# Performance work log

Hardware: AMD Instinct MI355X
Metric: run time of the kernel (lower is better)

## Reference

```python
import jax, jax.numpy as jnp
import numpy as np

N_BIT = 4
GROUP = 128
ALPHA_W = 1.0   # group_size > -1 forces weight alpha to 1.0
ALPHA_A = 0.9   # searched input alpha
TOKENS, D_IN, D_OUT = 2048, 2048, 2048


def _int_grid(n_bit):
    B = n_bit - 1
    v = [0.0] + [float(s * i) for i in range(1, 2 ** B) for s in (1, -1)]
    v = np.sort(np.asarray(v, np.float32)) * (32.0 / 2 ** B)
    return v


def _outlier_grid(n_bit, exp_bit=2, exp_base=5):
    B = n_bit - 1
    mant_bit = B - exp_bit
    vals = []
    for i in range(exp_base, exp_base + 2 ** exp_bit):
        for j in range(2 ** mant_bit):
            if i == exp_base and j == 0:
                continue
            v = 2.0 ** i * (1.0 + 2.0 ** (-mant_bit) * j)
            vals += [v, -v]
    return np.sort(np.asarray(vals, np.float32))


_QG = _int_grid(N_BIT)
MAX_Q = float(_QG.max())              # 28.0 for 4-bit int grid
MERGED_GRID = jnp.asarray(np.concatenate([_QG, _outlier_grid(N_BIT)]))  # [29]


def get_quant(x, alpha, group_size):
    """Faithful jax port of get_quant(): per-group scale, nearest merged-grid
    quantization, roll-based outlier/victim masking, fp16 dequant."""
    org_shape = x.shape
    if group_size == -2:
        t = x.reshape(-1)
        mean, std = t.mean(), t.std(ddof=1)
    else:
        t = x.reshape(-1, group_size) if group_size > 0 else x
        mean = t.mean(axis=1, keepdims=True)
        std = t.std(axis=1, ddof=1, keepdims=True)
    normal_max = jnp.maximum(jnp.abs(mean + 3 * std), jnp.abs(mean - 3 * std))
    scales = normal_max * alpha / MAX_Q
    # nearest grid point over merged quant+outlier grid (the chunk loop in the
    # original is memory-chunking only; math is identical done whole)
    labels = jnp.argmin(jnp.abs((t / scales)[..., None] - MERGED_GRID), axis=-1)
    qf = MERGED_GRID[labels].reshape(-1)
    # victim masking: outliers (|q|>32) steal their paired neighbor's slot
    mask = jnp.abs(qf) > 32.0
    victim_odd = jnp.roll(mask, 1).at[::2].set(False)
    victim_even = jnp.roll(mask & ~victim_odd, -1).at[1::2].set(False)
    qf = jnp.where(victim_odd | victim_even, 0.0, qf)
    if group_size >= -1:
        qf = qf.reshape(t.shape)
    deq = (qf * scales).astype(jnp.float16)
    return deq.reshape(org_shape)


def setup_inputs() -> dict:
    key = jax.random.key(0)
    k1, k2 = jax.random.split(key)
    x = jax.random.normal(k1, (TOKENS, D_IN), dtype=jnp.float32)
    weight = jax.random.normal(k2, (D_OUT, D_IN), dtype=jnp.float32) * 0.02
    return {"x": x, "weight": weight}


def reference(x, weight):
    # runtime path of OliVe_Linear.forward (post-calibration), group_size=128
    w_deq = get_quant(weight, ALPHA_W, GROUP).astype(jnp.float32)
    x_deq = get_quant(x, ALPHA_A, GROUP).astype(jnp.float32)
    return x_deq @ w_deq.T  # [tokens, out_features]
```

## Files before the change

kernel.cpp:

```cpp
#include <hip/hip_runtime.h>
#include <hip/hip_fp16.h>
#include <stdint.h>

#define TOKENS 2048
#define DIM    2048
#define GROUP  128
#define NGK    16

typedef _Float16 half_t;
typedef __attribute__((ext_vector_type(4)))  _Float16 f16x4;
typedef __attribute__((ext_vector_type(8)))  _Float16 f16x8;
typedef __attribute__((ext_vector_type(4)))  int   i32x4;
typedef __attribute__((ext_vector_type(16))) int   i32x16;
typedef __attribute__((ext_vector_type(4)))  float f32x4;
typedef __attribute__((ext_vector_type(16))) float f32x16;


__device__ __forceinline__ float group32_sum(float v) {
#pragma unroll
  for (int off = 16; off > 0; off >>= 1)
    v += __shfl_xor(v, off, 64);
  return v;
}

__device__ __forceinline__ float nearest_q4(float u) {
  float qi = fminf(fmaxf(rintf(u), -7.f), 7.f);
  float a = fabsf(u);
  float m = a <= 14.f ? 12.f : a <= 20.f ? 16.f : a <= 28.f ? 24.f
          : a <= 40.f ? 32.f : a <= 56.f ? 48.f : a <= 80.f ? 64.f : 96.f;
  float qo = copysignf(m, u);
  return (fabsf(u - qo) < fabsf(u - qi)) ? qo : qi;
}

__global__ __launch_bounds__(256) void quant2_kernel(
    const float* __restrict__ x, const float* __restrict__ w,
    int8_t* __restrict__ q8,
    half_t* __restrict__ ssxT,
    half_t* __restrict__ sswT) {
  const int wid  = threadIdx.x >> 6;
  const int lane = threadIdx.x & 63;
  const int l    = lane & 31;
  const int g    = blockIdx.x * 8 + wid * 2 + (lane >> 5);
  const int NG1  = TOKENS * DIM / GROUP;

  const float alpha = (g < NG1) ? 0.9f : 1.0f;
  const float* src  = (g < NG1) ? x : w;
  const int grow    = (g < NG1) ? g : g - NG1;
  const size_t sbase = (size_t)grow * GROUP + l * 4;

  const float4 v = *reinterpret_cast<const float4*>(src + sbase);

  const float mean = group32_sum(v.x + v.y + v.z + v.w) * (1.0f / 128.0f);
  const float d0 = v.x - mean, d1 = v.y - mean, d2 = v.z - mean, d3 = v.w - mean;
  const float var = group32_sum(d0 * d0 + d1 * d1 + d2 * d2 + d3 * d3) *
                    (1.0f / 127.0f);
  const float scale = (fabsf(mean) + 3.0f * sqrtf(var)) * alpha / 28.0f;
  const float rs4 = 0.25f / scale;

  float q0 = nearest_q4(v.x * rs4);
  float q1 = nearest_q4(v.y * rs4);
  float q2 = nearest_q4(v.z * rs4);
  float q3 = nearest_q4(v.w * rs4);
  if (fabsf(q0) > 8.0f)      q1 = 0.0f;
  else if (fabsf(q1) > 8.0f) q0 = 0.0f;
  if (fabsf(q2) > 8.0f)      q3 = 0.0f;
  else if (fabsf(q3) > 8.0f) q2 = 0.0f;

  const int p = ((int)q0 & 255) | (((int)q1 & 255) << 8) |
                (((int)q2 & 255) << 16) | (((int)q3 & 255) << 24);
  reinterpret_cast<int*>(q8)[(size_t)g * 32 + l] = p;

  if (l == 0) {
    const half_t ss = (half_t)(4.0f * scale);
    if (g < NG1) ssxT[(grow & 15) * 2048 + (grow >> 4)] = ss;
    else         sswT[(grow & 15) * 2048 + (grow >> 4)] = ss;
  }
}


__device__ __forceinline__ void gload_lds16(const int8_t* g, char* l) {
  __builtin_amdgcn_global_load_lds(
      (__attribute__((address_space(1))) uint32_t*)g,
      (__attribute__((address_space(3))) uint32_t*)l, 16, 0, 0);
}

__global__ __launch_bounds__(256, 2) void gemm_kernel(
    const int8_t* __restrict__ Aq, const int8_t* __restrict__ Bq,
    const half_t* __restrict__ ssxT, const half_t* __restrict__ sswT,
    float* __restrict__ C) {
  __shared__ char lds_raw[3 * 24576 + 6144];
  half_t* ssx_l = (half_t*)(lds_raw + 73728);
  half_t* ssw_l = (half_t*)(lds_raw + 73728 + 4096);

  const int tid  = threadIdx.x;
  const int lane = tid & 63;
  const int wid  = tid >> 6;
  const int wr   = wid >> 1;
  const int wc   = wid & 1;
  const int r31  = lane & 31;
  const int hi   = lane >> 5;

  const int bid = blockIdx.x;
  const int c   = bid & 7;
  const int idx = bid >> 3;
  const int bm  = ((c & 3) << 2) + (idx >> 4);
  const int bn  = ((c >> 2) << 4) + (idx & 15);

  const int8_t* gA = Aq + (size_t)(bm * 128) * DIM;
  const int8_t* gB = Bq + (size_t)(bn * 64) * DIM;

  auto stage = [&](char* buf, int g) {
#pragma unroll
    for (int i = 0; i < 4; ++i) {
      int P   = (i * 256 + tid) * 16;
      int row = P >> 7;
      int cb  = (P & 127) ^ ((row & 7) << 4);
      gload_lds16(gA + (size_t)row * DIM + g * 128 + cb, buf + P);
    }
#pragma unroll
    for (int i = 0; i < 2; ++i) {
      int P   = (i * 256 + tid) * 16;
      int row = P >> 7;
      int cb  = (P & 127) ^ ((row & 7) << 4);
      gload_lds16(gB + (size_t)row * DIM + g * 128 + cb, buf + 16384 + P);
    }
  };

  {
    int f = tid * 8;
    *reinterpret_cast<f16x8*>(&ssx_l[f]) =
        *reinterpret_cast<const f16x8*>(&ssxT[(f >> 7) * 2048 + bm * 128 + (f & 127)]);
  }
  if (tid < 128) {
    int f = tid * 8;
    *reinterpret_cast<f16x8*>(&ssw_l[f]) =
        *reinterpret_cast<const f16x8*>(&sswT[(f >> 6) * 2048 + bn * 64 + (f & 63)]);
  }
  __syncthreads();

  f32x16 accf[2] = {};
  const i32x16 zacc = {};

  auto compute = [&](const char* buf, int gk) {
    const char* cA = buf;
    const char* cB = buf + 16384;
    i32x16 acci[2];
#pragma unroll
    for (int ks = 0; ks < 4; ++ks) {
      const int cb = ks * 32 + hi * 16;
      i32x4 af[2], bf;
#pragma unroll
      for (int mt = 0; mt < 2; ++mt) {
        int row = wr * 64 + mt * 32 + r31;
        int pc  = cb ^ ((row & 7) << 4);
        af[mt] = *reinterpret_cast<const i32x4*>(cA + (row << 7) + pc);
      }
      {
        int row = wc * 32 + r31;
        int pc  = cb ^ ((row & 7) << 4);
        bf = *reinterpret_cast<const i32x4*>(cB + (row << 7) + pc);
      }
      __builtin_amdgcn_s_setprio(1);
#pragma unroll
      for (int mt = 0; mt < 2; ++mt)
        acci[mt] = __builtin_amdgcn_mfma_i32_32x32x32_i8(
            af[mt], bf, ks == 0 ? zacc : acci[mt], 0, 0, 0);
      __builtin_amdgcn_s_setprio(0);
    }
    const float sw = (float)ssw_l[gk * 64 + wc * 32 + r31];
#pragma unroll
    for (int mt = 0; mt < 2; ++mt)
#pragma unroll
      for (int q = 0; q < 4; ++q) {
        f16x4 sxh = *reinterpret_cast<const f16x4*>(
            &ssx_l[gk * 128 + wr * 64 + mt * 32 + 8 * q + 4 * hi]);
#pragma unroll
        for (int e = 0; e < 4; ++e)
          accf[mt][q * 4 + e] +=
              (float)sxh[e] * (sw * (float)acci[mt][q * 4 + e]);
      }
  };

  char* S0 = lds_raw;
  char* S1 = lds_raw + 24576;
  char* S2 = lds_raw + 49152;

  stage(S0, 0);
  stage(S1, 1);

  auto iter = [&](int j, const char* cbuf, char* sbuf) {
    if (j <= 13) {
      stage(sbuf, j + 2);
      asm volatile("s_waitcnt vmcnt(12)" ::: "memory");
    } else if (j == 14) {
      asm volatile("s_waitcnt vmcnt(6)" ::: "memory");
    } else {
      asm volatile("s_waitcnt vmcnt(0)" ::: "memory");
    }
    __builtin_amdgcn_s_barrier();
    compute(cbuf, j);
    __builtin_amdgcn_s_barrier();
  };

  for (int t = 0; t < 12; t += 3) {
    iter(t + 0, S0, S2);
    iter(t + 1, S1, S0);
    iter(t + 2, S2, S1);
  }
  iter(12, S0, S2);
  iter(13, S1, S0);
  iter(14, S2, S1);
  iter(15, S0, S2);

  const int crow0 = bm * 128 + wr * 64 + 4 * hi;
  const int ccol  = bn * 64 + wc * 32 + r31;
#pragma unroll
  for (int mt = 0; mt < 2; ++mt)
#pragma unroll
    for (int r = 0; r < 16; ++r) {
      int row = crow0 + mt * 32 + (r & 3) + 8 * (r >> 2);
      C[(size_t)row * DIM + ccol] = accf[mt][r];
    }
}


extern "C" void kernel_launch(void* const* d_in, const int* in_sizes, int n_in,
                              void* d_out, int out_size, void* d_ws,
                              size_t ws_size, hipStream_t stream) {
  const float* x = (const float*)d_in[0];
  const float* w = (const float*)d_in[1];
  float* out = (float*)d_out;

  int8_t* qx   = (int8_t*)d_ws;
  int8_t* qw   = qx + (size_t)TOKENS * DIM;
  half_t* ssxT = (half_t*)(qw + (size_t)DIM * DIM);
  half_t* sswT = ssxT + NGK * 2048;

  const int ngroups = 2 * TOKENS * DIM / GROUP;
  quant2_kernel<<<ngroups / 8, 256, 0, stream>>>(x, w, qx, ssxT, sswT);

  gemm_kernel<<<512, 256, 0, stream>>>(qx, qw, ssxT, sswT, out);
}
```

Measured before the change: 35.51 us.

## Single barrier per K-step in GEMM pipeline and fp32 weight scales

Restructures the triple-buffered K loop so each iteration waits for the current stage, barriers once, then issues the next stage's loads before computing. This drops the trailing barrier per iteration. The first global-to-LDS stages are also issued before the scale preload so they overlap it. Weight scales are now stored and loaded as fp32 instead of fp16, which adds precision and LDS usage. Reusing the buffer after a single barrier relies on the three-buffer rotation keeping the buffer being overwritten distinct from the one still being read.

```diff
diff --git a/kernel.cpp b/kernel.cpp
--- a/kernel.cpp
+++ b/kernel.cpp
@@ -36,7 +36,7 @@
     const float* __restrict__ x, const float* __restrict__ w,
     int8_t* __restrict__ q8,
     half_t* __restrict__ ssxT,
-    half_t* __restrict__ sswT) {
+    float* __restrict__ sswT) {
   const int wid  = threadIdx.x >> 6;
   const int lane = threadIdx.x & 63;
   const int l    = lane & 31;
@@ -71,8 +71,8 @@
   reinterpret_cast<int*>(q8)[(size_t)g * 32 + l] = p;
 
   if (l == 0) {
-    const half_t ss = (half_t)(4.0f * scale);
-    if (g < NG1) ssxT[(grow & 15) * 2048 + (grow >> 4)] = ss;
+    const float ss = 4.0f * scale;
+    if (g < NG1) ssxT[(grow & 15) * 2048 + (grow >> 4)] = (half_t)ss;
     else         sswT[(grow & 15) * 2048 + (grow >> 4)] = ss;
   }
 }
@@ -86,11 +86,11 @@
 
 __global__ __launch_bounds__(256, 2) void gemm_kernel(
     const int8_t* __restrict__ Aq, const int8_t* __restrict__ Bq,
-    const half_t* __restrict__ ssxT, const half_t* __restrict__ sswT,
+    const half_t* __restrict__ ssxT, const float* __restrict__ sswT,
     float* __restrict__ C) {
-  __shared__ char lds_raw[3 * 24576 + 6144];
+  __shared__ char lds_raw[3 * 24576 + 8192];
   half_t* ssx_l = (half_t*)(lds_raw + 73728);
-  half_t* ssw_l = (half_t*)(lds_raw + 73728 + 4096);
+  float*  ssw_l = (float*)(lds_raw + 73728 + 4096);
 
   const int tid  = threadIdx.x;
   const int lane = tid & 63;
@@ -126,15 +126,22 @@
     }
   };
 
+  char* S0 = lds_raw;
+  char* S1 = lds_raw + 24576;
+  char* S2 = lds_raw + 49152;
+
+  stage(S0, 0);
+  stage(S1, 1);
+
   {
     int f = tid * 8;
     *reinterpret_cast<f16x8*>(&ssx_l[f]) =
         *reinterpret_cast<const f16x8*>(&ssxT[(f >> 7) * 2048 + bm * 128 + (f & 127)]);
   }
-  if (tid < 128) {
-    int f = tid * 8;
-    *reinterpret_cast<f16x8*>(&ssw_l[f]) =
-        *reinterpret_cast<const f16x8*>(&sswT[(f >> 6) * 2048 + bn * 64 + (f & 63)]);
+  {
+    int f = tid * 4;
+    *reinterpret_cast<f32x4*>(&ssw_l[f]) =
+        *reinterpret_cast<const f32x4*>(&sswT[(f >> 6) * 2048 + bn * 64 + (f & 63)]);
   }
   __syncthreads();
 
@@ -167,7 +174,7 @@
             af[mt], bf, ks == 0 ? zacc : acci[mt], 0, 0, 0);
       __builtin_amdgcn_s_setprio(0);
     }
-    const float sw = (float)ssw_l[gk * 64 + wc * 32 + r31];
+    const float sw = ssw_l[gk * 64 + wc * 32 + r31];
 #pragma unroll
     for (int mt = 0; mt < 2; ++mt)
 #pragma unroll
@@ -181,36 +188,21 @@
       }
   };
 
-  char* S0 = lds_raw;
-  char* S1 = lds_raw + 24576;
-  char* S2 = lds_raw + 49152;
-
-  stage(S0, 0);
-  stage(S1, 1);
-
   auto iter = [&](int j, const char* cbuf, char* sbuf) {
-    if (j <= 13) {
-      stage(sbuf, j + 2);
-      asm volatile("s_waitcnt vmcnt(12)" ::: "memory");
-    } else if (j == 14) {
-      asm volatile("s_waitcnt vmcnt(6)" ::: "memory");
-    } else {
-      asm volatile("s_waitcnt vmcnt(0)" ::: "memory");
-    }
+    asm volatile("s_waitcnt vmcnt(6)" ::: "memory");
     __builtin_amdgcn_s_barrier();
+    if (j <= 13) stage(sbuf, j + 2);
     compute(cbuf, j);
-    __builtin_amdgcn_s_barrier();
   };
 
-  for (int t = 0; t < 12; t += 3) {
+  for (int t = 0; t < 15; t += 3) {
     iter(t + 0, S0, S2);
     iter(t + 1, S1, S0);
     iter(t + 2, S2, S1);
   }
-  iter(12, S0, S2);
-  iter(13, S1, S0);
-  iter(14, S2, S1);
-  iter(15, S0, S2);
+  asm volatile("s_waitcnt vmcnt(0)" ::: "memory");
+  __builtin_amdgcn_s_barrier();
+  compute(S0, 15);
 
   const int crow0 = bm * 128 + wr * 64 + 4 * hi;
   const int ccol  = bn * 64 + wc * 32 + r31;
@@ -234,7 +226,7 @@
   int8_t* qx   = (int8_t*)d_ws;
   int8_t* qw   = qx + (size_t)TOKENS * DIM;
   half_t* ssxT = (half_t*)(qw + (size_t)DIM * DIM);
-  half_t* sswT = ssxT + NGK * 2048;
+  float*  sswT = (float*)(ssxT + NGK * 2048);
 
   const int ngroups = 2 * TOKENS * DIM / GROUP;
   quant2_kernel<<<ngroups / 8, 256, 0, stream>>>(x, w, qx, ssxT, sswT);
```

New measurement: 34.85 us. About the same (-1.8%).
